# Kernel optimization log

Measured on AMD Instinct MI355X. Metric: run time of the kernel, lower is better.

Reference implementation:

```python
import jax, jax.numpy as jnp
import numpy as np

B, T, C, H = 8, 2048, 1024, 64  # batch, seq_len(block_size), embedding_size, head_size


def setup_inputs() -> dict:
    key = jax.random.key(0)
    kx, kk, kq, kv = jax.random.split(key, 4)
    x = jax.random.normal(kx, (B, T, C), dtype=jnp.float32)
    # nn.Linear(C, H, bias=False) weights, stored as [in, out] for x @ W
    s = 1.0 / np.sqrt(C)
    Wk = jax.random.uniform(kk, (C, H), dtype=jnp.float32, minval=-s, maxval=s)
    Wq = jax.random.uniform(kq, (C, H), dtype=jnp.float32, minval=-s, maxval=s)
    Wv = jax.random.uniform(kv, (C, H), dtype=jnp.float32, minval=-s, maxval=s)
    return {"x": x, "Wk": Wk, "Wq": Wq, "Wv": Wv}


def reference(x, Wk, Wq, Wv):
    Bx, Tx, Cx = x.shape
    k = jnp.einsum('btc,ch->bth', x, Wk)
    q = jnp.einsum('btc,ch->bth', x, Wq)
    v = jnp.einsum('btc,ch->bth', x, Wv)
    # NOTE: original scales by embedding dim C ** -0.5, not head_size
    scores = jnp.einsum('bth,bsh->bts', q, k) * (Cx ** -0.5)  # [B,T,T]
    causal = jnp.tril(jnp.ones((Tx, Tx), dtype=bool))
    scores = jnp.where(causal, scores, -jnp.inf)
    attn = jax.nn.softmax(scores, axis=-1)
    # dropout is identity in eval/deterministic mode
    out = jnp.einsum('bts,bsh->bth', attn, v)  # [B,T,H]
    return out
```

## Files before the change

kernel.cpp:

```cpp
#include <hip/hip_runtime.h>
#include <hip/hip_bf16.h>
#include <math.h>


#define BT 16384
#define TSEQ 2048
#define XST 72

typedef __attribute__((ext_vector_type(8))) __bf16 bf16x8;
typedef __attribute__((ext_vector_type(8))) unsigned short ushort8;
typedef __attribute__((ext_vector_type(4))) float floatx4;

#define MFMA16(a, b, c) __builtin_amdgcn_mfma_f32_16x16x32_bf16( \
    __builtin_bit_cast(bf16x8, (a)), __builtin_bit_cast(bf16x8, (b)), (c), 0, 0, 0)

__device__ inline unsigned short f2bf(float f) {
  unsigned u = __builtin_bit_cast(unsigned, f);
  u += 0x7FFFu + ((u >> 16) & 1u);
  return (unsigned short)(u >> 16);
}
__device__ inline float bf2f(unsigned short s) {
  return __builtin_bit_cast(float, (unsigned)s << 16);
}
__device__ inline unsigned long long pack4bf(floatx4 f) {
  return (unsigned long long)f2bf(f[0]) | ((unsigned long long)f2bf(f[1]) << 16) |
         ((unsigned long long)f2bf(f[2]) << 32) | ((unsigned long long)f2bf(f[3]) << 48);
}

__global__ __launch_bounds__(256) void wt2_kernel(
    const float* __restrict__ Wq, const float* __restrict__ Wk,
    const float* __restrict__ Wv, unsigned short* __restrict__ Wt2) {
  __shared__ float ls[64][65];
  const int m = blockIdx.x >> 4;
  const int kci = blockIdx.x & 15;
  const int c0 = kci << 6;
  const float* __restrict__ W = (m == 0) ? Wq : (m == 1) ? Wk : Wv;
  const int tid = threadIdx.x;
#pragma unroll
  for (int i = 0; i < 16; ++i) {
    int idx = tid + (i << 8);
    int cl = idx >> 6, h = idx & 63;
    ls[cl][h] = W[(c0 + cl) * 64 + h];
  }
  __syncthreads();
  const int w = tid >> 6, lane = tid & 63;
  const int quad = lane >> 4, l16 = lane & 15;
  const int nt = (m << 2) + w;
#pragma unroll
  for (int half = 0; half < 2; ++half) {
    ushort8 t;
#pragma unroll
    for (int j = 0; j < 8; ++j)
      t[j] = f2bf(ls[(half << 5) + (quad << 3) + j][(w << 4) + l16]);
    *(ushort8*)(Wt2 + ((size_t)(((nt << 4) + kci) * 2 + half) << 9) +
                (lane << 3)) = t;
  }
}

__global__ __launch_bounds__(256) void qkv_mfma(
    const float* __restrict__ x, const unsigned short* __restrict__ Wt2,
    unsigned short* __restrict__ Qf, unsigned short* __restrict__ Kf,
    unsigned short* __restrict__ Vf) {
  __shared__ unsigned short region[4][16 * XST];
  __shared__ float red[2][12][64][4];

  const int tid = threadIdx.x;
  const int w = tid >> 6, lane = tid & 63;
  const int quad = lane >> 4, l16 = lane & 15;
  const int r0 = blockIdx.x << 4;
  const float* __restrict__ xw = x + (size_t)r0 * 1024 + (w << 8);
  const int srow = lane >> 4, scol = (lane & 15) << 2;

  floatx4 acc[12];
#pragma unroll
  for (int i = 0; i < 12; ++i) acc[i] = (floatx4){0.f, 0.f, 0.f, 0.f};

  floatx4 pf[2][4];
#pragma unroll
  for (int i = 0; i < 4; ++i)
    pf[0][i] = *(const floatx4*)(xw + (size_t)((i << 2) + srow) * 1024 + scol);
#pragma unroll
  for (int i = 0; i < 4; ++i)
    pf[1][i] = *(const floatx4*)(xw + (size_t)((i << 2) + srow) * 1024 + 64 + scol);

  unsigned short* buf = &region[w][0];
#pragma unroll
  for (int it = 0; it < 4; ++it) {
#pragma unroll
    for (int i = 0; i < 4; ++i)
      *(unsigned long long*)&buf[((i << 2) + srow) * XST + scol] =
          pack4bf(pf[it & 1][i]);
    if (it < 2) {
#pragma unroll
      for (int i = 0; i < 4; ++i)
        pf[it & 1][i] = *(const floatx4*)(xw + (size_t)((i << 2) + srow) * 1024 +
                                          ((it + 2) << 6) + scol);
    }
    ushort8 a0 = *(const ushort8*)&buf[l16 * XST + (quad << 3)];
    ushort8 a1 = *(const ushort8*)&buf[l16 * XST + 32 + (quad << 3)];
    const int kci = (w << 2) + it;
    const unsigned short* bbase = Wt2 + ((size_t)kci << 10) + ((size_t)lane << 3);
#pragma unroll
    for (int nt = 0; nt < 12; ++nt) {
      const unsigned short* bp = bbase + ((size_t)nt << 14);
      ushort8 b0 = *(const ushort8*)bp;
      ushort8 b1 = *(const ushort8*)(bp + 512);
      acc[nt] = MFMA16(a0, b0, acc[nt]);
      acc[nt] = MFMA16(a1, b1, acc[nt]);
    }
  }

  if (w == 1) {
#pragma unroll
    for (int nt = 0; nt < 12; ++nt) *(floatx4*)&red[0][nt][lane][0] = acc[nt];
  } else if (w == 3) {
#pragma unroll
    for (int nt = 0; nt < 12; ++nt) *(floatx4*)&red[1][nt][lane][0] = acc[nt];
  }
  __syncthreads();
  if (w == 0) {
#pragma unroll
    for (int nt = 0; nt < 12; ++nt) acc[nt] += *(const floatx4*)&red[0][nt][lane][0];
  } else if (w == 2) {
#pragma unroll
    for (int nt = 0; nt < 12; ++nt) acc[nt] += *(const floatx4*)&red[1][nt][lane][0];
  }
  __syncthreads();
  if (w == 2) {
#pragma unroll
    for (int nt = 0; nt < 12; ++nt) *(floatx4*)&red[0][nt][lane][0] = acc[nt];
  }
  __syncthreads();
  unsigned short* qs = &region[0][0];
  unsigned short* ks = qs + 16 * XST;
  unsigned short* vt = ks + 16 * XST;
  if (w == 0) {
#pragma unroll
    for (int nt = 0; nt < 12; ++nt) acc[nt] += *(const floatx4*)&red[0][nt][lane][0];
#pragma unroll
    for (int nt = 0; nt < 4; ++nt)
#pragma unroll
      for (int r = 0; r < 4; ++r)
        qs[((quad << 2) + r) * XST + (nt << 4) + l16] = f2bf(acc[nt][r]);
#pragma unroll
    for (int nt = 4; nt < 8; ++nt)
#pragma unroll
      for (int r = 0; r < 4; ++r)
        ks[((quad << 2) + r) * XST + ((nt - 4) << 4) + l16] = f2bf(acc[nt][r]);
#pragma unroll
    for (int nt = 8; nt < 12; ++nt)
#pragma unroll
      for (int r = 0; r < 4; ++r)
        vt[(((nt - 8) << 4) + l16) * 24 + (quad << 2) + r] = f2bf(acc[nt][r]);
  }
  __syncthreads();

  const int b = r0 >> 11;
  const int r16 = (r0 & 2047) >> 4;
  const int st = (r0 & 2047) >> 6;
  const int ntK = (r0 >> 4) & 3;
  const int khV = (r0 >> 5) & 1;
  const int q0v = (r0 >> 3) & 3;
  if (w == 0) {
#pragma unroll
    for (int kh = 0; kh < 2; ++kh) {
      ushort8 t = *(const ushort8*)&qs[l16 * XST + (kh << 5) + (quad << 3)];
      *(ushort8*)(Qf + ((((size_t)b * 128 + r16) * 2 + kh) << 9) + (lane << 3)) = t;
    }
  } else if (w == 1) {
#pragma unroll
    for (int kh = 0; kh < 2; ++kh) {
      ushort8 t = *(const ushort8*)&ks[l16 * XST + (kh << 5) + (quad << 3)];
      *(ushort8*)(Kf + ((((size_t)(b * 32 + st) * 4 + ntK) * 2 + kh) << 9) +
                  (lane << 3)) = t;
    }
  } else {
    if ((quad >> 1) == (q0v >> 1)) {
#pragma unroll
      for (int sub = 0; sub < 2; ++sub) {
        const int ntE = ((w - 2) << 1) + sub;
        ushort8 t = *(const ushort8*)&vt[((ntE << 4) + l16) * 24 +
                                         ((quad - q0v) << 3)];
        *(ushort8*)(Vf + ((((size_t)(b * 32 + st) * 4 + ntE) * 2 + khV) << 9) +
                    (lane << 3)) = t;
      }
    }
  }
}

__global__ __launch_bounds__(128) void attn_part(
    const unsigned short* __restrict__ Qf, const unsigned short* __restrict__ Kf,
    const unsigned short* __restrict__ Vf, float* __restrict__ part) {
  __shared__ unsigned short Pw[2][16 * XST];

  const int tid = threadIdx.x;
  const int w = tid >> 6, lane = tid & 63;
  const int quad = lane >> 4, l16 = lane & 15;
  const int b = blockIdx.x / 288;
  const int rem = blockIdx.x - b * 288;
  const int e = rem >> 1, half = rem & 1;
  int g = 0;
#pragma unroll
  for (int gg = 1; gg < 8; ++gg) g += (e >= 2 * gg * (gg + 1)) ? 1 : 0;
  const int rem2 = e - 2 * g * (g + 1);
  const int qt = (g << 2) + rem2 / (g + 1);
  const int ch = rem2 - (rem2 / (g + 1)) * (g + 1);
  const int s0 = ch << 2;
  const int s1 = min(s0 + 4, qt + 1);
  const int rg = (half << 1) + w;
  const int r16 = (qt << 2) + rg;

  const unsigned short* qbase =
      Qf + ((((size_t)b * 128 + r16) * 2) << 9) + (lane << 3);
  ushort8 qf0 = *(const ushort8*)qbase;
  ushort8 qf1 = *(const ushort8*)(qbase + 512);

  floatx4 acc[4], lacc;
#pragma unroll
  for (int nt = 0; nt < 4; ++nt) acc[nt] = (floatx4){0.f, 0.f, 0.f, 0.f};
  lacc = (floatx4){0.f, 0.f, 0.f, 0.f};
  const ushort8 ones = {0x3F80, 0x3F80, 0x3F80, 0x3F80,
                        0x3F80, 0x3F80, 0x3F80, 0x3F80};

#define KVIDX(ss, nt, kh) \
  (((((size_t)(b * 32 + (ss)) << 2) + (nt)) * 2 + (kh)) << 9)

  ushort8 bk[4][2];
#pragma unroll
  for (int nt = 0; nt < 4; ++nt)
#pragma unroll
    for (int kh = 0; kh < 2; ++kh)
      bk[nt][kh] = *(const ushort8*)(Kf + KVIDX(s0, nt, kh) + (lane << 3));

  for (int s = s0; s < s1; ++s) {
    const int sn = (s + 1 < s1) ? s + 1 : s;
    ushort8 bv[4][2];
#pragma unroll
    for (int nt = 0; nt < 4; ++nt)
#pragma unroll
      for (int kh = 0; kh < 2; ++kh)
        bv[nt][kh] = *(const ushort8*)(Vf + KVIDX(s, nt, kh) + (lane << 3));
    ushort8 bkn[4][2];
#pragma unroll
    for (int nt = 0; nt < 4; ++nt)
#pragma unroll
      for (int kh = 0; kh < 2; ++kh)
        bkn[nt][kh] = *(const ushort8*)(Kf + KVIDX(sn, nt, kh) + (lane << 3));

    floatx4 sf[4];
#pragma unroll
    for (int nt = 0; nt < 4; ++nt) {
      sf[nt] = (floatx4){0.f, 0.f, 0.f, 0.f};
      sf[nt] = MFMA16(qf0, bk[nt][0], sf[nt]);
      sf[nt] = MFMA16(qf1, bk[nt][1], sf[nt]);
    }

    const bool diag = (s == qt);
    const int qrow = (rg << 4) + (quad << 2);
#pragma unroll
    for (int nt = 0; nt < 4; ++nt) {
      const int keyl = (nt << 4) + l16;
#pragma unroll
      for (int r = 0; r < 4; ++r) {
        float ev = __expf(sf[nt][r] * 0.03125f);
        if (diag && keyl > ((qt << 6) - (qt << 6)) + qrow + r) ev = 0.f;
        Pw[w][((quad << 2) + r) * XST + keyl] = f2bf(ev);
      }
    }

#pragma unroll
    for (int kh = 0; kh < 2; ++kh) {
      ushort8 pa = *(const ushort8*)&Pw[w][l16 * XST + (kh << 5) + (quad << 3)];
      lacc = MFMA16(pa, ones, lacc);
#pragma unroll
      for (int nt = 0; nt < 4; ++nt) acc[nt] = MFMA16(pa, bv[nt][kh], acc[nt]);
    }
#pragma unroll
    for (int nt = 0; nt < 4; ++nt) {
      bk[nt][0] = bkn[nt][0];
      bk[nt][1] = bkn[nt][1];
    }
  }
#undef KVIDX

  float* slot = part + (size_t)(b * 144 + e) * 2112;
  if (l16 == 0) {
#pragma unroll
    for (int r = 0; r < 4; ++r) slot[(rg << 4) + (quad << 2) + r] = lacc[r];
  }
  unsigned short* op = (unsigned short*)(slot + 64);
#pragma unroll
  for (int nt = 0; nt < 4; ++nt)
#pragma unroll
    for (int r = 0; r < 4; ++r)
      op[((rg << 4) + (quad << 2) + r) * 64 + (nt << 4) + l16] = f2bf(acc[nt][r]);
}

__global__ __launch_bounds__(256) void attn_combine(
    const float* __restrict__ part, float* __restrict__ out) {
  const int rh = blockIdx.x & 1;
  const int bqt = blockIdx.x >> 1;
  const int b = bqt >> 5, qt = bqt & 31;
  const int tid = threadIdx.x;
  const int row = (rh << 5) + (tid >> 3);
  const int hseg = (tid & 7) << 3;
  const int g = qt >> 2;
  const int nch = g + 1;
  const int ebase = 2 * g * (g + 1) + (qt & 3) * (g + 1);

  float l = 0.f;
  float ov[8];
#pragma unroll
  for (int i = 0; i < 8; ++i) ov[i] = 0.f;
  for (int c = 0; c < nch; ++c) {
    const float* slot = part + (size_t)(b * 144 + ebase + c) * 2112;
    l += slot[row];
    ushort8 o0 = *(const ushort8*)((const unsigned short*)(slot + 64) +
                                   row * 64 + hseg);
#pragma unroll
    for (int i = 0; i < 8; ++i) ov[i] += bf2f(o0[i]);
  }
  const float inv = 1.f / l;
  float* o = out + ((size_t)(b * TSEQ + (qt << 6) + row)) * 64 + hseg;
#pragma unroll
  for (int i = 0; i < 8; ++i) o[i] = ov[i] * inv;
}

extern "C" void kernel_launch(void* const* d_in, const int* in_sizes, int n_in,
                              void* d_out, int out_size, void* d_ws, size_t ws_size,
                              hipStream_t stream) {
  const float* x  = (const float*)d_in[0];
  const float* Wk = (const float*)d_in[1];
  const float* Wq = (const float*)d_in[2];
  const float* Wv = (const float*)d_in[3];

  unsigned short* Qfw = (unsigned short*)d_ws;
  unsigned short* Kfw = Qfw + (size_t)BT * 64;
  unsigned short* Vfw = Kfw + (size_t)BT * 64;
  unsigned short* Wt2 = Vfw + (size_t)BT * 64;
  float* part = (float*)(Wt2 + 3 * 64 * 1024);

  wt2_kernel<<<48, 256, 0, stream>>>(Wq, Wk, Wv, Wt2);
  qkv_mfma<<<1024, 256, 0, stream>>>(x, Wt2, Qfw, Kfw, Vfw);
  attn_part<<<2304, 128, 0, stream>>>(Qfw, Kfw, Vfw, part);
  attn_combine<<<512, 256, 0, stream>>>(part, (float*)d_out);
}
```

Measured before the change: 143.7 us.

## Retile QKV projection to 64-row blocks with LDS-staged weights and double buffering

Rewrites the QKV projection kernel so each 512-thread block computes 64 rows across the full K dimension. Weight fragments are staged into LDS with global_load_lds, and the x tiles are converted to bf16 in LDS, both double-buffered along K. This replaces the old scheme of 16-row blocks with split-K across warps, which reloaded weights from global memory per block and needed a shared-memory reduction. It is meant to cut redundant weight traffic and remove the reduction, at the cost of fewer blocks (256) and larger LDS use, which may lower occupancy.

```diff
diff --git a/kernel.cpp b/kernel.cpp
--- a/kernel.cpp
+++ b/kernel.cpp
@@ -25,6 +25,19 @@
 __device__ inline unsigned long long pack4bf(floatx4 f) {
   return (unsigned long long)f2bf(f[0]) | ((unsigned long long)f2bf(f[1]) << 16) |
          ((unsigned long long)f2bf(f[2]) << 32) | ((unsigned long long)f2bf(f[3]) << 48);
+}
+__device__ inline ushort8 pack8bf(floatx4 a, floatx4 b) {
+  ushort8 t;
+#pragma unroll
+  for (int i = 0; i < 4; ++i) t[i] = f2bf(a[i]);
+#pragma unroll
+  for (int i = 0; i < 4; ++i) t[4 + i] = f2bf(b[i]);
+  return t;
+}
+__device__ inline void glds16(const unsigned short* g, unsigned short* l) {
+  __builtin_amdgcn_global_load_lds(
+      (const __attribute__((address_space(1))) unsigned int*)g,
+      (__attribute__((address_space(3))) unsigned int*)l, 16, 0, 0);
 }
 
 __global__ __launch_bounds__(256) void wt2_kernel(
@@ -57,134 +70,137 @@
   }
 }
 
-__global__ __launch_bounds__(256) void qkv_mfma(
+#define BB0 9216
+#define BBS 12288
+#define XBS 4608
+
+__global__ __launch_bounds__(512) void qkv_mfma(
     const float* __restrict__ x, const unsigned short* __restrict__ Wt2,
     unsigned short* __restrict__ Qf, unsigned short* __restrict__ Kf,
     unsigned short* __restrict__ Vf) {
-  __shared__ unsigned short region[4][16 * XST];
-  __shared__ float red[2][12][64][4];
+  __shared__ unsigned short smem[33792];
 
   const int tid = threadIdx.x;
   const int w = tid >> 6, lane = tid & 63;
   const int quad = lane >> 4, l16 = lane & 15;
-  const int r0 = blockIdx.x << 4;
-  const float* __restrict__ xw = x + (size_t)r0 * 1024 + (w << 8);
-  const int srow = lane >> 4, scol = (lane & 15) << 2;
-
-  floatx4 acc[12];
-#pragma unroll
-  for (int i = 0; i < 12; ++i) acc[i] = (floatx4){0.f, 0.f, 0.f, 0.f};
-
-  floatx4 pf[2][4];
-#pragma unroll
-  for (int i = 0; i < 4; ++i)
-    pf[0][i] = *(const floatx4*)(xw + (size_t)((i << 2) + srow) * 1024 + scol);
-#pragma unroll
-  for (int i = 0; i < 4; ++i)
-    pf[1][i] = *(const floatx4*)(xw + (size_t)((i << 2) + srow) * 1024 + 64 + scol);
-
-  unsigned short* buf = &region[w][0];
-#pragma unroll
-  for (int it = 0; it < 4; ++it) {
-#pragma unroll
-    for (int i = 0; i < 4; ++i)
-      *(unsigned long long*)&buf[((i << 2) + srow) * XST + scol] =
-          pack4bf(pf[it & 1][i]);
-    if (it < 2) {
-#pragma unroll
-      for (int i = 0; i < 4; ++i)
-        pf[it & 1][i] = *(const floatx4*)(xw + (size_t)((i << 2) + srow) * 1024 +
-                                          ((it + 2) << 6) + scol);
-    }
-    ushort8 a0 = *(const ushort8*)&buf[l16 * XST + (quad << 3)];
-    ushort8 a1 = *(const ushort8*)&buf[l16 * XST + 32 + (quad << 3)];
-    const int kci = (w << 2) + it;
-    const unsigned short* bbase = Wt2 + ((size_t)kci << 10) + ((size_t)lane << 3);
-#pragma unroll
-    for (int nt = 0; nt < 12; ++nt) {
-      const unsigned short* bp = bbase + ((size_t)nt << 14);
-      ushort8 b0 = *(const ushort8*)bp;
-      ushort8 b1 = *(const ushort8*)(bp + 512);
-      acc[nt] = MFMA16(a0, b0, acc[nt]);
-      acc[nt] = MFMA16(a1, b1, acc[nt]);
-    }
-  }
-
-  if (w == 1) {
-#pragma unroll
-    for (int nt = 0; nt < 12; ++nt) *(floatx4*)&red[0][nt][lane][0] = acc[nt];
-  } else if (w == 3) {
-#pragma unroll
-    for (int nt = 0; nt < 12; ++nt) *(floatx4*)&red[1][nt][lane][0] = acc[nt];
+  const int wr = w >> 2, wn = w & 3;
+  const int r0 = blockIdx.x << 6;
+
+  const int xrow = (w << 3) + (lane >> 3);
+  const int xcol = (lane & 7) << 3;
+  const float* __restrict__ xp = x + (size_t)(r0 + xrow) * 1024 + xcol;
+  const int xw_u16 = xrow * XST + xcol;
+
+  floatx4 acc[2][3];
+#pragma unroll
+  for (int rt = 0; rt < 2; ++rt)
+#pragma unroll
+    for (int n = 0; n < 3; ++n) acc[rt][n] = (floatx4){0.f, 0.f, 0.f, 0.f};
+
+  floatx4 pf[2][2];
+
+#pragma unroll
+  for (int i = 0; i < 3; ++i) {
+    const int f = 3 * w + i;
+    glds16(Wt2 + ((size_t)(((f >> 1) << 4) * 2 + (f & 1)) << 9) + (lane << 3),
+           &smem[BB0 + (f << 9)]);
+  }
+  pf[0][0] = *(const floatx4*)(xp);
+  pf[0][1] = *(const floatx4*)(xp + 4);
+  pf[1][0] = *(const floatx4*)(xp + 64);
+  pf[1][1] = *(const floatx4*)(xp + 68);
+  *(ushort8*)&smem[xw_u16] = pack8bf(pf[0][0], pf[0][1]);
+  asm volatile("s_waitcnt lgkmcnt(0)");
+  __builtin_amdgcn_sched_barrier(0);
+  __builtin_amdgcn_s_barrier();
+  __builtin_amdgcn_sched_barrier(0);
+
+#pragma unroll
+  for (int c = 0; c < 16; ++c) {
+    const int cur = c & 1, nxt = cur ^ 1;
+    if (c + 1 < 16) {
+#pragma unroll
+      for (int i = 0; i < 3; ++i) {
+        const int f = 3 * w + i;
+        glds16(Wt2 + ((size_t)((((f >> 1) << 4) + (c + 1)) * 2 + (f & 1)) << 9) +
+                   (lane << 3),
+               &smem[BB0 + nxt * BBS + (f << 9)]);
+      }
+      *(ushort8*)&smem[nxt * XBS + xw_u16] =
+          pack8bf(pf[(c + 1) & 1][0], pf[(c + 1) & 1][1]);
+    }
+    if (c + 2 < 16) {
+      pf[c & 1][0] = *(const floatx4*)(xp + ((c + 2) << 6));
+      pf[c & 1][1] = *(const floatx4*)(xp + ((c + 2) << 6) + 4);
+    }
+    __builtin_amdgcn_sched_barrier(0);
+
+    ushort8 af[2][2];
+#pragma unroll
+    for (int rt = 0; rt < 2; ++rt)
+#pragma unroll
+      for (int h = 0; h < 2; ++h)
+        af[rt][h] = *(const ushort8*)&smem[cur * XBS +
+            ((wr << 5) + (rt << 4) + l16) * XST + (h << 5) + (quad << 3)];
+    ushort8 bfr[3][2];
+#pragma unroll
+    for (int n = 0; n < 3; ++n)
+#pragma unroll
+      for (int h = 0; h < 2; ++h)
+        bfr[n][h] = *(const ushort8*)&smem[BB0 + cur * BBS +
+            ((((3 * wn + n) << 1) + h) << 9) + (lane << 3)];
+#pragma unroll
+    for (int h = 0; h < 2; ++h)
+#pragma unroll
+      for (int rt = 0; rt < 2; ++rt)
+#pragma unroll
+        for (int n = 0; n < 3; ++n)
+          acc[rt][n] = MFMA16(af[rt][h], bfr[n][h], acc[rt][n]);
+
+    __builtin_amdgcn_sched_barrier(0);
+    if (c < 14) { asm volatile("s_waitcnt vmcnt(2)"); }
+    else        { asm volatile("s_waitcnt vmcnt(0)"); }
+    asm volatile("s_waitcnt lgkmcnt(0)");
+    __builtin_amdgcn_sched_barrier(0);
+    __builtin_amdgcn_s_barrier();
+    __builtin_amdgcn_sched_barrier(0);
+  }
+
+#pragma unroll
+  for (int n = 0; n < 3; ++n) {
+    const int nt = 3 * wn + n;
+    const int m = nt >> 2, hg = nt & 3;
+#pragma unroll
+    for (int rt = 0; rt < 2; ++rt) {
+      const int rowb = (wr << 5) + (rt << 4) + (quad << 2);
+      if (m < 2) {
+#pragma unroll
+        for (int r = 0; r < 4; ++r)
+          smem[m * XBS + (rowb + r) * XST + (hg << 4) + l16] =
+              f2bf(acc[rt][n][r]);
+      } else {
+        *(unsigned long long*)&smem[2 * XBS + ((hg << 4) + l16) * XST + rowb] =
+            pack4bf(acc[rt][n]);
+      }
+    }
   }
   __syncthreads();
-  if (w == 0) {
-#pragma unroll
-    for (int nt = 0; nt < 12; ++nt) acc[nt] += *(const floatx4*)&red[0][nt][lane][0];
-  } else if (w == 2) {
-#pragma unroll
-    for (int nt = 0; nt < 12; ++nt) acc[nt] += *(const floatx4*)&red[1][nt][lane][0];
-  }
-  __syncthreads();
-  if (w == 2) {
-#pragma unroll
-    for (int nt = 0; nt < 12; ++nt) *(floatx4*)&red[0][nt][lane][0] = acc[nt];
-  }
-  __syncthreads();
-  unsigned short* qs = &region[0][0];
-  unsigned short* ks = qs + 16 * XST;
-  unsigned short* vt = ks + 16 * XST;
-  if (w == 0) {
-#pragma unroll
-    for (int nt = 0; nt < 12; ++nt) acc[nt] += *(const floatx4*)&red[0][nt][lane][0];
-#pragma unroll
-    for (int nt = 0; nt < 4; ++nt)
-#pragma unroll
-      for (int r = 0; r < 4; ++r)
-        qs[((quad << 2) + r) * XST + (nt << 4) + l16] = f2bf(acc[nt][r]);
-#pragma unroll
-    for (int nt = 4; nt < 8; ++nt)
-#pragma unroll
-      for (int r = 0; r < 4; ++r)
-        ks[((quad << 2) + r) * XST + ((nt - 4) << 4) + l16] = f2bf(acc[nt][r]);
-#pragma unroll
-    for (int nt = 8; nt < 12; ++nt)
-#pragma unroll
-      for (int r = 0; r < 4; ++r)
-        vt[(((nt - 8) << 4) + l16) * 24 + (quad << 2) + r] = f2bf(acc[nt][r]);
-  }
-  __syncthreads();
-
-  const int b = r0 >> 11;
-  const int r16 = (r0 & 2047) >> 4;
-  const int st = (r0 & 2047) >> 6;
-  const int ntK = (r0 >> 4) & 3;
-  const int khV = (r0 >> 5) & 1;
-  const int q0v = (r0 >> 3) & 3;
-  if (w == 0) {
-#pragma unroll
-    for (int kh = 0; kh < 2; ++kh) {
-      ushort8 t = *(const ushort8*)&qs[l16 * XST + (kh << 5) + (quad << 3)];
-      *(ushort8*)(Qf + ((((size_t)b * 128 + r16) * 2 + kh) << 9) + (lane << 3)) = t;
-    }
-  } else if (w == 1) {
-#pragma unroll
-    for (int kh = 0; kh < 2; ++kh) {
-      ushort8 t = *(const ushort8*)&ks[l16 * XST + (kh << 5) + (quad << 3)];
-      *(ushort8*)(Kf + ((((size_t)(b * 32 + st) * 4 + ntK) * 2 + kh) << 9) +
-                  (lane << 3)) = t;
-    }
-  } else {
-    if ((quad >> 1) == (q0v >> 1)) {
-#pragma unroll
-      for (int sub = 0; sub < 2; ++sub) {
-        const int ntE = ((w - 2) << 1) + sub;
-        ushort8 t = *(const ushort8*)&vt[((ntE << 4) + l16) * 24 +
-                                         ((quad - q0v) << 3)];
-        *(ushort8*)(Vf + ((((size_t)(b * 32 + st) * 4 + ntE) * 2 + khV) << 9) +
-                    (lane << 3)) = t;
-      }
-    }
+
+  const int b = blockIdx.x >> 5, st = blockIdx.x & 31;
+#pragma unroll
+  for (int i = 0; i < 3; ++i) {
+    const int f = w * 3 + i;
+    const int m = f >> 3, idx = f & 7, grp = idx >> 1, kh = idx & 1;
+    ushort8 t = *(const ushort8*)&smem[m * XBS + ((grp << 4) + l16) * XST +
+                                       (kh << 5) + (quad << 3)];
+    unsigned short* dst;
+    if (m == 0)
+      dst = Qf + (((size_t)(b * 128 + (st << 2) + grp) * 2 + kh) << 9);
+    else if (m == 1)
+      dst = Kf + (((size_t)((b * 32 + st) * 4 + grp) * 2 + kh) << 9);
+    else
+      dst = Vf + (((size_t)((b * 32 + st) * 4 + grp) * 2 + kh) << 9);
+    *(ushort8*)(dst + (lane << 3)) = t;
   }
 }
 
@@ -341,7 +357,7 @@
   float* part = (float*)(Wt2 + 3 * 64 * 1024);
 
   wt2_kernel<<<48, 256, 0, stream>>>(Wq, Wk, Wv, Wt2);
-  qkv_mfma<<<1024, 256, 0, stream>>>(x, Wt2, Qfw, Kfw, Vfw);
+  qkv_mfma<<<256, 512, 0, stream>>>(x, Wt2, Qfw, Kfw, Vfw);
   attn_part<<<2304, 128, 0, stream>>>(Qfw, Kfw, Vfw, part);
   attn_combine<<<512, 256, 0, stream>>>(part, (float*)d_out);
 }
```

New measurement: 132.5 us. 1.08x faster.
